# Kernel optimization log

Hardware: AMD Instinct MI355X
Metric: run time of the kernel (lower is better)

Reference implementation:

```python
import jax, jax.numpy as jnp
import numpy as np

ALPHA = 0.1        # axis_aligned_projection threshold
NEG_INF = -1e30    # large negative used for masking (softmax-equivalent to -inf)


def axis_aligned_projection(x, alpha=ALPHA):
    x_abs = jnp.abs(x)
    max_vals = jnp.max(x_abs, axis=-1, keepdims=True)
    axis_weights = jnp.where(x_abs >= alpha * max_vals, x_abs, 0.0)
    return axis_weights * jnp.sign(x)


def setup_inputs() -> dict:
    key = jax.random.key(0)
    kq, kk, kv = jax.random.split(key, 3)
    B, L, H, E = 4, 2048, 8, 64
    S, D = L, E
    queries = jax.random.normal(kq, (B, L, H, E), dtype=jnp.float32)
    keys = jax.random.normal(kk, (B, S, H, E), dtype=jnp.float32)
    values = jax.random.normal(kv, (B, S, H, D), dtype=jnp.float32)
    # TriangularCausalMask: True strictly above the diagonal -> masked out
    causal = jnp.triu(jnp.ones((L, S), dtype=jnp.bool_), k=1)
    attn_mask = jnp.broadcast_to(causal[None, None], (B, 1, L, S))
    return {"queries": queries, "keys": keys, "values": values, "attn_mask": attn_mask}


def reference(queries, keys, values, attn_mask):
    B, L, H, E = queries.shape
    scale = 1.0 / jnp.sqrt(jnp.float32(E))
    q = axis_aligned_projection(queries)
    k = axis_aligned_projection(keys)
    # [B,H,L,S] dense scores (the module materializes the full matrix)
    scores = jnp.einsum('blhe,bshe->bhls', q, k)
    scores = jnp.where(attn_mask, NEG_INF, scores)
    A = jax.nn.softmax(scale * scores, axis=-1)  # dropout is identity in eval mode
    V = jnp.einsum('bhls,bshd->blhd', A, values)
    return V
```

## Files before the change

### kernel.cpp

```cpp
#include <hip/hip_runtime.h>
#include <hip/hip_bf16.h>
#include <stdint.h>

#define B_ 4
#define L_ 2048
#define H_ 8
#define E_ 64
#define ALPHA 0.1f
#define LOG2E 1.44269504088896f
#define QSCALE (0.125f * LOG2E)
#define KSTR 72

typedef float f32x4 __attribute__((ext_vector_type(4)));
typedef short bf16x8 __attribute__((ext_vector_type(8)));
typedef short bf16x4 __attribute__((ext_vector_type(4)));
typedef uint32_t u32;
typedef unsigned short u16;
typedef u32 u32x2 __attribute__((ext_vector_type(2)));

__device__ __forceinline__ u16 f2bf(float f) {
    u32 x = __builtin_bit_cast(u32, f);
    u32 r = x + 0x7fffu + ((x >> 16) & 1u);
    return (u16)(r >> 16);
}

__device__ __forceinline__ u32 pk2bf(float a, float b) {
    u32 ua = __builtin_bit_cast(u32, a) + 0x8000u;
    u32 ub = __builtin_bit_cast(u32, b) + 0x8000u;
    return (ua >> 16) | (ub & 0xffff0000u);
}

__device__ __forceinline__ f32x4 mfma16x16x16bf16(bf16x4 a, bf16x4 b, f32x4 c) {
#if __has_builtin(__builtin_amdgcn_mfma_f32_16x16x16bf16_1k)
    return __builtin_amdgcn_mfma_f32_16x16x16bf16_1k(a, b, c, 0, 0, 0);
#elif __has_builtin(__builtin_amdgcn_mfma_f32_16x16x16_bf16)
    return __builtin_amdgcn_mfma_f32_16x16x16_bf16(a, b, c, 0, 0, 0);
#else
    f32x4 d;
    asm volatile("v_mfma_f32_16x16x16_bf16 %0, %1, %2, %3"
                 : "=v"(d) : "v"(a), "v"(b), "v"(c));
    return d;
#endif
}

__device__ __forceinline__ void dma16(const u16* g, u16* l) {
    __builtin_amdgcn_global_load_lds(
        (const __attribute__((address_space(1))) void*)g,
        (__attribute__((address_space(3))) void*)l, 16, 0, 0);
}

__global__ __launch_bounds__(256) void prep_kernel(const float* __restrict__ qin,
                                                   const float* __restrict__ kin,
                                                   const float* __restrict__ vin,
                                                   u16* __restrict__ qp,
                                                   u16* __restrict__ kp,
                                                   u16* __restrict__ vt) {
    __shared__ u16 tile[64][66];
    if (blockIdx.x < 4096) {
        const int RG = (B_ * L_ * H_) / 8;
        int wave = threadIdx.x >> 6, lane = threadIdx.x & 63;
        int g = blockIdx.x * 4 + wave;
        const float* src;
        u16* dst;
        int gr, ostr;
        float sc;
        if (g < RG) { src = qin; dst = qp; gr = g; sc = QSCALE; ostr = 64; }
        else        { src = kin; dst = kp; gr = g - RG; sc = 1.0f; ostr = KSTR; }

        int rig = lane >> 3;
        int c = (lane & 7) * 4;
        int row = gr * 8 + rig;

        const float* rp = src + (size_t)row * 64;
        float4 v0 = *(const float4*)(rp + c);
        float4 v1 = *(const float4*)(rp + c + 32);
        float f[8] = {v0.x, v0.y, v0.z, v0.w, v1.x, v1.y, v1.z, v1.w};

        float mx = 0.f;
#pragma unroll
        for (int i = 0; i < 8; ++i) mx = fmaxf(mx, fabsf(f[i]));
#pragma unroll
        for (int m = 1; m < 8; m <<= 1) mx = fmaxf(mx, __shfl_xor(mx, m));
        float thr = ALPHA * mx;

        u16 o[8];
#pragma unroll
        for (int i = 0; i < 8; ++i)
            o[i] = (fabsf(f[i]) >= thr) ? f2bf(f[i] * sc) : (u16)0;

        int b = row >> 14;
        int l = (row >> 3) & (L_ - 1);
        int h = row & 7;
        u16* orow = dst + ((size_t)(b * H_ + h) * L_ + l) * ostr;
        uint2 p0 = {(u32)o[0] | ((u32)o[1] << 16), (u32)o[2] | ((u32)o[3] << 16)};
        uint2 p1 = {(u32)o[4] | ((u32)o[5] << 16), (u32)o[6] | ((u32)o[7] << 16)};
        *(uint2*)(orow + c) = p0;
        *(uint2*)(orow + c + 32) = p1;
    } else {
        int bx = blockIdx.x - 4096;
        int bh = bx >> 5, sblk = bx & 31;
        int b = bh >> 3, h = bh & 7;
        int t = threadIdx.x;
        int s0 = sblk * 64;

#pragma unroll
        for (int p = 0; p < 2; ++p) {
            int sl = p * 32 + (t >> 3);
            int c = (t & 7) * 4;
            const float* rp = vin + (((size_t)(b * L_ + s0 + sl)) * H_ + h) * 64;
            float4 a = *(const float4*)(rp + c);
            float4 bb = *(const float4*)(rp + c + 32);
            u32* d0 = (u32*)&tile[sl][c];
            d0[0] = (u32)f2bf(a.x) | ((u32)f2bf(a.y) << 16);
            d0[1] = (u32)f2bf(a.z) | ((u32)f2bf(a.w) << 16);
            u32* d1 = (u32*)&tile[sl][c + 32];
            d1[0] = (u32)f2bf(bb.x) | ((u32)f2bf(bb.y) << 16);
            d1[1] = (u32)f2bf(bb.z) | ((u32)f2bf(bb.w) << 16);
        }
        __syncthreads();
#pragma unroll
        for (int p = 0; p < 2; ++p) {
            int d = p * 32 + (t >> 3);
            int sc2 = (t & 7) * 8;
            u16 o[8];
#pragma unroll
            for (int i = 0; i < 8; ++i) o[i] = tile[sc2 + i][d];
            uint4 val;
            val.x = (u32)o[0] | ((u32)o[1] << 16);
            val.y = (u32)o[2] | ((u32)o[3] << 16);
            val.z = (u32)o[4] | ((u32)o[5] << 16);
            val.w = (u32)o[6] | ((u32)o[7] << 16);
            *(uint4*)(vt + ((size_t)(bh * 32 + sblk) * 64 + d) * KSTR + sc2) = val;
        }
    }
}

__global__ __launch_bounds__(256, 4) void flash_kernel(const u16* __restrict__ Qp,
                                                       const u16* __restrict__ Kp,
                                                       const u16* __restrict__ Vt,
                                                       float* __restrict__ out,
                                                       float* __restrict__ pO,
                                                       float* __restrict__ pL) {
    __shared__ u16 kbuf[2][64 * KSTR];
    __shared__ u16 vbuf[2][64 * KSTR];
    int t = threadIdx.x;
    int wave = t >> 6, lane = t & 63;
    int bh = blockIdx.x & 31;
    int o5 = blockIdx.x >> 5;
    int lo = lane & 15, quad = lane >> 4;
    int b = bh >> 3, h = bh & 7;

    int group, t0, t1, slot;
    bool diag;
    if (o5 < 16)       { group = 16 + o5; t0 = 0;  t1 = 15;    diag = false; slot = 0; }
    else if (o5 == 16) { group = 31;      t0 = 16; t1 = 31;    diag = true;  slot = 1; }
    else if (o5 == 17) { group = 15;      t0 = 0;  t1 = 15;    diag = true;  slot = -1; }
    else {
        int op = o5 - 18;
        int lam = 15 - (op >> 1);
        if (!(op & 1)) { group = 15 + lam; t0 = 16; t1 = 15 + lam; diag = true; slot = 1; }
        else           { group = lam - 1;  t0 = 0;  t1 = lam - 1;  diag = true; slot = -1; }
    }
    int q0 = group * 64 + wave * 16;

    const u16* kTiles = Kp + (size_t)bh * L_ * KSTR;
    const u16* vTiles = Vt + (size_t)bh * 32 * 64 * KSTR;

    auto stage = [&](int tile, int buf) {
        const u16* kg = kTiles + (size_t)tile * 64 * KSTR;
        const u16* vg = vTiles + (size_t)tile * 64 * KSTR;
        u16* kl = kbuf[buf];
        u16* vl = vbuf[buf];
        for (int i = wave; i < 18; i += 4) {
            if (i < 9) dma16(kg + i * 512 + lane * 8, kl + i * 512);
            else       dma16(vg + (i - 9) * 512 + lane * 8, vl + (i - 9) * 512);
        }
    };

    const u16* qbase = Qp + ((size_t)bh * L_ + q0 + lo) * 64 + quad * 8;
    bf16x8 aQ0 = *(const bf16x8*)(qbase);
    bf16x8 aQ1 = *(const bf16x8*)(qbase + 32);

    f32x4 o[4];
#pragma unroll
    for (int ni = 0; ni < 4; ++ni) o[ni] = (f32x4){0.f, 0.f, 0.f, 0.f};
    float ls = 0.f;

    auto frag_proc = [&](const u16* ks, const u16* vs, int sub, bool dg) {
        bf16x8 k0 = *(const bf16x8*)(ks + (sub * 16 + lo) * KSTR + quad * 8);
        bf16x8 k1 = *(const bf16x8*)(ks + (sub * 16 + lo) * KSTR + 32 + quad * 8);
        f32x4 S = {0.f, 0.f, 0.f, 0.f};
        S = __builtin_amdgcn_mfma_f32_16x16x32_bf16(k0, aQ0, S, 0, 0, 0);
        S = __builtin_amdgcn_mfma_f32_16x16x32_bf16(k1, aQ1, S, 0, 0, 0);

        bf16x4 vf[4];
#pragma unroll
        for (int ni = 0; ni < 4; ++ni)
            vf[ni] = *(const bf16x4*)(vs + (ni * 16 + lo) * KSTR + sub * 16 + quad * 4);

        float P[4];
#pragma unroll
        for (int r = 0; r < 4; ++r) {
            float e = __builtin_amdgcn_exp2f(S[r]);
            P[r] = (dg && (quad * 4 + r > lo)) ? 0.f : e;
        }
        ls += (P[0] + P[1]) + (P[2] + P[3]);
        u32x2 pk = {pk2bf(P[0], P[1]), pk2bf(P[2], P[3])};
        bf16x4 aP = __builtin_bit_cast(bf16x4, pk);
#pragma unroll
        for (int ni = 0; ni < 4; ++ni)
            o[ni] = mfma16x16x16bf16(aP, vf[ni], o[ni]);
    };

    stage(t0, 0);
    __syncthreads();

    for (int kt = t0; kt < t1; ++kt) {
        int cur = (kt - t0) & 1;
        stage(kt + 1, cur ^ 1);
        const u16* ks = kbuf[cur];
        const u16* vs = vbuf[cur];
#pragma unroll
        for (int sub = 0; sub < 4; ++sub) frag_proc(ks, vs, sub, false);
        __syncthreads();
    }

    {
        int cur = (t1 - t0) & 1;
        const u16* ks = kbuf[cur];
        const u16* vs = vbuf[cur];
        if (diag) {
            for (int sub = 0; sub < wave; ++sub) frag_proc(ks, vs, sub, false);
            frag_proc(ks, vs, wave, true);
        } else {
#pragma unroll
            for (int sub = 0; sub < 4; ++sub) frag_proc(ks, vs, sub, false);
        }
    }

    ls += __shfl_xor(ls, 16);
    ls += __shfl_xor(ls, 32);
    if (slot < 0) {
#pragma unroll
        for (int r = 0; r < 4; ++r) {
            float lr = __shfl(ls, quad * 4 + r);
            float inv = 1.0f / lr;
            int q = q0 + quad * 4 + r;
            float* ob = out + (((size_t)(b * L_ + q)) * H_ + h) * 64 + lo;
            ob[0]  = o[0][r] * inv;
            ob[16] = o[1][r] * inv;
            ob[32] = o[2][r] * inv;
            ob[48] = o[3][r] * inv;
        }
    } else {
        int gi = group - 16;
        size_t sbase = ((size_t)(bh * 16 + gi) * 2 + slot);
        float* po = pO + sbase * 4096 + (wave * 16 + quad * 4) * 64 + lo;
#pragma unroll
        for (int r = 0; r < 4; ++r) {
            po[r * 64 + 0]  = o[0][r];
            po[r * 64 + 16] = o[1][r];
            po[r * 64 + 32] = o[2][r];
            po[r * 64 + 48] = o[3][r];
        }
        if (quad == 0) pL[sbase * 64 + wave * 16 + lo] = ls;
    }
}

__global__ __launch_bounds__(256) void combine_kernel(const float* __restrict__ pO,
                                                      const float* __restrict__ pL,
                                                      float* __restrict__ out) {
    __shared__ float linv[64];
    int bh = blockIdx.x & 31, gi = blockIdx.x >> 5;
    int b = bh >> 3, h = bh & 7;
    int group = 16 + gi;
    int t = threadIdx.x;
    size_t sb = (size_t)(bh * 16 + gi) * 2;
    if (t < 64) linv[t] = 1.0f / (pL[sb * 64 + t] + pL[(sb + 1) * 64 + t]);
    __syncthreads();
    const float4* O1 = (const float4*)(pO + sb * 4096);
    const float4* O2 = (const float4*)(pO + (sb + 1) * 4096);
#pragma unroll
    for (int k = 0; k < 4; ++k) {
        int f4 = t * 4 + k;
        int f = f4 * 4;
        int ql = f >> 6, d = f & 63;
        float4 a = O1[f4], c = O2[f4];
        float s = linv[ql];
        float4 r = {(a.x + c.x) * s, (a.y + c.y) * s, (a.z + c.z) * s, (a.w + c.w) * s};
        int q = group * 64 + ql;
        *(float4*)(out + (((size_t)(b * L_ + q)) * H_ + h) * 64 + d) = r;
    }
}

extern "C" void kernel_launch(void* const* d_in, const int* in_sizes, int n_in,
                              void* d_out, int out_size, void* d_ws, size_t ws_size,
                              hipStream_t stream) {
    const float* q = (const float*)d_in[0];
    const float* k = (const float*)d_in[1];
    const float* v = (const float*)d_in[2];
    float* out = (float*)d_out;

    const size_t QSZ = (size_t)B_ * H_ * L_ * 64;
    const size_t KSZ = (size_t)B_ * H_ * L_ * KSTR;
    u16* qp = (u16*)d_ws;
    u16* kp = qp + QSZ;
    u16* vt = kp + KSZ;
    float* pO = (float*)(vt + KSZ);
    float* pL = pO + (size_t)32 * 16 * 2 * 4096;

    prep_kernel<<<5120, 256, 0, stream>>>(q, k, v, qp, kp, vt);
    flash_kernel<<<1536, 256, 0, stream>>>(qp, kp, vt, out, pO, pL);
    combine_kernel<<<512, 256, 0, stream>>>(pO, pL, out);
}
```

Before: 173.9 us.

## Double query tile to 128 rows per block with 8 waves sharing K/V tiles

```diff
diff --git a/kernel.cpp b/kernel.cpp
--- a/kernel.cpp
+++ b/kernel.cpp
@@ -135,7 +135,7 @@
     }
 }
 
-__global__ __launch_bounds__(256, 4) void flash_kernel(const u16* __restrict__ Qp,
+__global__ __launch_bounds__(512, 8) void flash_kernel(const u16* __restrict__ Qp,
                                                        const u16* __restrict__ Kp,
                                                        const u16* __restrict__ Vt,
                                                        float* __restrict__ out,
@@ -151,17 +151,15 @@
     int b = bh >> 3, h = bh & 7;
 
     int group, t0, t1, slot;
-    bool diag;
-    if (o5 < 16)       { group = 16 + o5; t0 = 0;  t1 = 15;    diag = false; slot = 0; }
-    else if (o5 == 16) { group = 31;      t0 = 16; t1 = 31;    diag = true;  slot = 1; }
-    else if (o5 == 17) { group = 15;      t0 = 0;  t1 = 15;    diag = true;  slot = -1; }
+    if (o5 < 8) { group = 8 + o5; t0 = 0; t1 = 15; slot = 0; }
     else {
-        int op = o5 - 18;
-        int lam = 15 - (op >> 1);
-        if (!(op & 1)) { group = 15 + lam; t0 = 16; t1 = 15 + lam; diag = true; slot = 1; }
-        else           { group = lam - 1;  t0 = 0;  t1 = lam - 1;  diag = true; slot = -1; }
-    }
-    int q0 = group * 64 + wave * 16;
+        int p = o5 - 8;
+        if ((p & 1) == 0) { group = 7 - (p >> 1);  t0 = 0;  t1 = 15 - p; slot = -1; }
+        else              { group = 15 - (p >> 1); t0 = 16; t1 = 32 - p; slot = 1; }
+    }
+    int q0 = group * 128 + wave * 16;
+    int dt = 2 * group + (wave >> 2);
+    int subd = wave & 3;
 
     const u16* kTiles = Kp + (size_t)bh * L_ * KSTR;
     const u16* vTiles = Vt + (size_t)bh * 32 * 64 * KSTR;
@@ -171,7 +169,7 @@
         const u16* vg = vTiles + (size_t)tile * 64 * KSTR;
         u16* kl = kbuf[buf];
         u16* vl = vbuf[buf];
-        for (int i = wave; i < 18; i += 4) {
+        for (int i = wave; i < 18; i += 8) {
             if (i < 9) dma16(kg + i * 512 + lane * 8, kl + i * 512);
             else       dma16(vg + (i - 9) * 512 + lane * 8, vl + (i - 9) * 512);
         }
@@ -215,27 +213,19 @@
     stage(t0, 0);
     __syncthreads();
 
-    for (int kt = t0; kt < t1; ++kt) {
+    for (int kt = t0; kt <= t1; ++kt) {
         int cur = (kt - t0) & 1;
-        stage(kt + 1, cur ^ 1);
+        if (kt < t1) stage(kt + 1, cur ^ 1);
         const u16* ks = kbuf[cur];
         const u16* vs = vbuf[cur];
-#pragma unroll
-        for (int sub = 0; sub < 4; ++sub) frag_proc(ks, vs, sub, false);
-        __syncthreads();
-    }
-
-    {
-        int cur = (t1 - t0) & 1;
-        const u16* ks = kbuf[cur];
-        const u16* vs = vbuf[cur];
-        if (diag) {
-            for (int sub = 0; sub < wave; ++sub) frag_proc(ks, vs, sub, false);
-            frag_proc(ks, vs, wave, true);
-        } else {
+        if (kt < dt) {
 #pragma unroll
             for (int sub = 0; sub < 4; ++sub) frag_proc(ks, vs, sub, false);
-        }
+        } else if (kt == dt) {
+            for (int sub = 0; sub < subd; ++sub) frag_proc(ks, vs, sub, false);
+            frag_proc(ks, vs, subd, true);
+        }
+        if (kt < t1) __syncthreads();
     }
 
     ls += __shfl_xor(ls, 16);
@@ -253,9 +243,9 @@
             ob[48] = o[3][r] * inv;
         }
     } else {
-        int gi = group - 16;
-        size_t sbase = ((size_t)(bh * 16 + gi) * 2 + slot);
-        float* po = pO + sbase * 4096 + (wave * 16 + quad * 4) * 64 + lo;
+        int gi = group - 8;
+        size_t s = ((size_t)(bh * 8 + gi) * 2 + slot);
+        float* po = pO + s * 8192 + (wave * 16 + quad * 4) * 64 + lo;
 #pragma unroll
         for (int r = 0; r < 4; ++r) {
             po[r * 64 + 0]  = o[0][r];
@@ -263,32 +253,32 @@
             po[r * 64 + 32] = o[2][r];
             po[r * 64 + 48] = o[3][r];
         }
-        if (quad == 0) pL[sbase * 64 + wave * 16 + lo] = ls;
+        if (quad == 0) pL[s * 128 + wave * 16 + lo] = ls;
     }
 }
 
 __global__ __launch_bounds__(256) void combine_kernel(const float* __restrict__ pO,
                                                       const float* __restrict__ pL,
                                                       float* __restrict__ out) {
-    __shared__ float linv[64];
+    __shared__ float linv[128];
     int bh = blockIdx.x & 31, gi = blockIdx.x >> 5;
     int b = bh >> 3, h = bh & 7;
-    int group = 16 + gi;
+    int group = 8 + gi;
     int t = threadIdx.x;
-    size_t sb = (size_t)(bh * 16 + gi) * 2;
-    if (t < 64) linv[t] = 1.0f / (pL[sb * 64 + t] + pL[(sb + 1) * 64 + t]);
+    size_t sb = (size_t)(bh * 8 + gi) * 2;
+    if (t < 128) linv[t] = 1.0f / (pL[sb * 128 + t] + pL[(sb + 1) * 128 + t]);
     __syncthreads();
-    const float4* O1 = (const float4*)(pO + sb * 4096);
-    const float4* O2 = (const float4*)(pO + (sb + 1) * 4096);
-#pragma unroll
-    for (int k = 0; k < 4; ++k) {
-        int f4 = t * 4 + k;
+    const float4* O1 = (const float4*)(pO + sb * 8192);
+    const float4* O2 = (const float4*)(pO + (sb + 1) * 8192);
+#pragma unroll
+    for (int k = 0; k < 8; ++k) {
+        int f4 = k * 256 + t;
         int f = f4 * 4;
         int ql = f >> 6, d = f & 63;
         float4 a = O1[f4], c = O2[f4];
         float s = linv[ql];
         float4 r = {(a.x + c.x) * s, (a.y + c.y) * s, (a.z + c.z) * s, (a.w + c.w) * s};
-        int q = group * 64 + ql;
+        int q = group * 128 + ql;
         *(float4*)(out + (((size_t)(b * L_ + q)) * H_ + h) * 64 + d) = r;
     }
 }
@@ -307,9 +297,9 @@
     u16* kp = qp + QSZ;
     u16* vt = kp + KSZ;
     float* pO = (float*)(vt + KSZ);
-    float* pL = pO + (size_t)32 * 16 * 2 * 4096;
+    float* pL = pO + (size_t)32 * 8 * 2 * 8192;
 
     prep_kernel<<<5120, 256, 0, stream>>>(q, k, v, qp, kp, vt);
-    flash_kernel<<<1536, 256, 0, stream>>>(qp, kp, vt, out, pO, pL);
-    combine_kernel<<<512, 256, 0, stream>>>(pO, pL, out);
-}
+    flash_kernel<<<768, 512, 0, stream>>>(qp, kp, vt, out, pO, pL);
+    combine_kernel<<<256, 256, 0, stream>>>(pO, pL, out);
+}
```

Result: slower. 187.2 us (+7.7%).
